# Kernel optimization log

Measured on AMD Instinct MI355X. Metric: run time of the kernel, lower is better.

Reference implementation:

```python
import jax, jax.numpy as jnp
import numpy as np

N_NODES = 50000
N_EDGES = 800000
EMB = 2
HID = 128
DIM = 2
IN_SZ = 3 * DIM + 1 + EMB  # boids_ode: delta_pos, r, dpos_i, dpos_j, a_i
MAX_RADIUS = 0.1


def setup_inputs() -> dict:
    key = jax.random.key(0)
    ks = jax.random.split(key, 12)
    s = 0.05  # modest weight scale for numeric stability
    return {
        "pos": jax.random.uniform(ks[0], (N_NODES, DIM), dtype=jnp.float32),
        "vel": jax.random.normal(ks[1], (N_NODES, DIM), dtype=jnp.float32),
        "a": jax.random.normal(ks[2], (2, N_NODES, EMB), dtype=jnp.float32),
        "vnorm": jnp.ones((1,), dtype=jnp.float32),
        "w0": jax.random.normal(ks[3], (IN_SZ, HID), dtype=jnp.float32) * s,
        "b0": jnp.zeros((HID,), dtype=jnp.float32),
        "w1": jax.random.normal(ks[4], (HID, HID), dtype=jnp.float32) * s,
        "b1": jnp.zeros((HID,), dtype=jnp.float32),
        "w2": jax.random.normal(ks[5], (HID, HID), dtype=jnp.float32) * s,
        "b2": jnp.zeros((HID,), dtype=jnp.float32),
        "w3": jax.random.normal(ks[6], (HID, HID), dtype=jnp.float32) * s,
        "b3": jnp.zeros((HID,), dtype=jnp.float32),
        "w4": jax.random.normal(ks[7], (HID, 2), dtype=jnp.float32) * s,
        "b4": jnp.zeros((2,), dtype=jnp.float32),
        "edge_index": jax.random.randint(ks[8], (2, N_EDGES), 0, N_NODES, dtype=jnp.int64),
        "data_id": 1,
    }


def _mlp(x, w0, b0, w1, b1, w2, b2, w3, b3, w4, b4):
    # 5-layer MLP with ReLU between linear layers (lin_edge)
    h = jax.nn.relu(x @ w0 + b0)
    h = jax.nn.relu(h @ w1 + b1)
    h = jax.nn.relu(h @ w2 + b2)
    h = jax.nn.relu(h @ w3 + b3)
    return h @ w4 + b4


def reference(pos, vel, a, vnorm, w0, b0, w1, b1, w2, b2, w3, b3, w4, b4,
              edge_index, data_id):
    d_pos = vel / vnorm                     # [N, 2]
    emb = a[data_id]                        # [N, EMB] (cell_id = arange)
    dst = edge_index[0]
    src = edge_index[1]
    delta_pos = (pos[src] - pos[dst]) / MAX_RADIUS          # [E, 2]
    r = jnp.sqrt(jnp.sum(delta_pos * delta_pos, axis=1))    # [E] (already / max_r)
    # boids_ode message: (delta_pos, r, dpos_i, dpos_j, a_i)
    feats = jnp.concatenate(
        [delta_pos, r[:, None], d_pos[dst], d_pos[src], emb[dst]], axis=-1)
    msgs = _mlp(feats, w0, b0, w1, b1, w2, b2, w3, b3, w4, b4)  # [E, 2]
    out = jax.ops.segment_sum(msgs, dst, num_segments=pos.shape[0])  # aggr='add'
    return out
```

## Files before the change

kernel.cpp:

```cpp
#include <hip/hip_runtime.h>
#include <math.h>

typedef _Float16 f16;
typedef __fp16 h2 __attribute__((ext_vector_type(2)));
typedef f16 f16x8 __attribute__((ext_vector_type(8)));
typedef float f32x16 __attribute__((ext_vector_type(16)));

#define LW0 0
#define LW1 16384
#define LW2 32768
#define W0F 49152
#define W4F 51200
#define BIAS16 55296
#define LBIAS 49152
#define LDS_F16 49536

__global__ void zero_f32(float* __restrict__ p, int n) {
    int i = blockIdx.x * blockDim.x + threadIdx.x;
    if (i < n) p[i] = 0.0f;
}

__global__ void prep_weights(const float* __restrict__ w1, const float* __restrict__ w2,
                             const float* __restrict__ w3, const float* __restrict__ w0,
                             const float* __restrict__ b0, const float* __restrict__ b1,
                             const float* __restrict__ b2, const float* __restrict__ b3,
                             const float* __restrict__ w4, f16* __restrict__ ws) {
    int t = blockIdx.x * 256 + threadIdx.x;
    if (t < 49152) {
        int l = t >> 14, rem = t & 16383;
        int fb = rem >> 12, ks = (rem >> 9) & 7, lane = (rem >> 3) & 63, i = rem & 7;
        int g = lane >> 5, ln = lane & 31;
        int F = 32 * (ks >> 1) + (i & 3) + 8 * (2 * (ks & 1) + (i >> 2)) + 4 * g;
        const float* w = (l == 0) ? w1 : (l == 1) ? w2 : w3;
        ws[t] = (f16)w[F * 128 + 32 * fb + ln];
    } else if (t < 51200) {
        int rem = t - 49152;
        int fb = rem >> 9, lane = (rem >> 3) & 63, i = rem & 7;
        int g = lane >> 5, ln = lane & 31;
        int k = 8 * g + i;
        int f = 32 * fb + ln;
        float v = (k < 9) ? w0[k * 128 + f] : (k == 9 ? b0[f] : 0.0f);
        ws[t] = (f16)v;
    } else if (t < 55296) {
        int rem = t - 51200;
        int ks = rem >> 9, lane = (rem >> 3) & 63, i = rem & 7;
        int g = lane >> 5, ln = lane & 31;
        int F = 32 * (ks >> 1) + (i & 3) + 8 * (2 * (ks & 1) + (i >> 2)) + 4 * g;
        ws[t] = (ln < 2) ? (f16)w4[F * 2 + ln] : (f16)0;
    } else if (t < 55680) {
        int m = t - 55296;
        int i = m & 7, g = (m >> 3) & 1, half = (m >> 4) & 1, fb = (m >> 5) & 3, lm = m >> 7;
        const float* bl = (lm == 0) ? b1 : (lm == 1) ? b2 : b3;
        ws[t] = (f16)bl[32 * fb + (i & 3) + 8 * (2 * half + (i >> 2)) + 4 * g];
    }
}

#define MF(w, b, c) __builtin_amdgcn_mfma_f32_32x32x16_f16(w, b, c, 0, 0, 0)

#define ZACC(acc) { _Pragma("unroll") for (int r_ = 0; r_ < 16; ++r_) acc[r_] = 0.0f; }

#define PACKB(dst, acc, b) {                                                   \
    h2 z2; z2[0] = (__fp16)0; z2[1] = (__fp16)0;                               \
    h2 p0 = __builtin_elementwise_max(__builtin_amdgcn_cvt_pkrtz(acc[8*(b)+0], acc[8*(b)+1]), z2); \
    h2 p1 = __builtin_elementwise_max(__builtin_amdgcn_cvt_pkrtz(acc[8*(b)+2], acc[8*(b)+3]), z2); \
    h2 p2 = __builtin_elementwise_max(__builtin_amdgcn_cvt_pkrtz(acc[8*(b)+4], acc[8*(b)+5]), z2); \
    h2 p3 = __builtin_elementwise_max(__builtin_amdgcn_cvt_pkrtz(acc[8*(b)+6], acc[8*(b)+7]), z2); \
    dst[0]=p0[0]; dst[1]=p0[1]; dst[2]=p1[0]; dst[3]=p1[1];                    \
    dst[4]=p2[0]; dst[5]=p2[1]; dst[6]=p3[0]; dst[7]=p3[1]; }

#define PACKBB(dst, acc, b, bias) {                                            \
    h2 z2; z2[0] = (__fp16)0; z2[1] = (__fp16)0;                               \
    const h2* bp_ = (const h2*)&(bias);                                        \
    h2 p0 = __builtin_elementwise_max(__builtin_amdgcn_cvt_pkrtz(acc[8*(b)+0], acc[8*(b)+1]) + bp_[0], z2); \
    h2 p1 = __builtin_elementwise_max(__builtin_amdgcn_cvt_pkrtz(acc[8*(b)+2], acc[8*(b)+3]) + bp_[1], z2); \
    h2 p2 = __builtin_elementwise_max(__builtin_amdgcn_cvt_pkrtz(acc[8*(b)+4], acc[8*(b)+5]) + bp_[2], z2); \
    h2 p3 = __builtin_elementwise_max(__builtin_amdgcn_cvt_pkrtz(acc[8*(b)+6], acc[8*(b)+7]) + bp_[3], z2); \
    dst[0]=p0[0]; dst[1]=p0[1]; dst[2]=p1[0]; dst[3]=p1[1];                    \
    dst[4]=p2[0]; dst[5]=p2[1]; dst[6]=p3[0]; dst[7]=p3[1]; }

#define MIDFB(LBASE, lm, fb, B0,B1,B2,B3,B4,B5,B6,B7, O0, O1) {                \
    f32x16 acc; ZACC(acc);                                                     \
    const f16* wb = lds + (LBASE) + (fb) * 4096 + lane * 8;                    \
    f16x8 w;                                                                   \
    w = *(const f16x8*)(wb + 0*512); acc = MF(w, B0, acc);                     \
    w = *(const f16x8*)(wb + 1*512); acc = MF(w, B1, acc);                     \
    w = *(const f16x8*)(wb + 2*512); acc = MF(w, B2, acc);                     \
    w = *(const f16x8*)(wb + 3*512); acc = MF(w, B3, acc);                     \
    w = *(const f16x8*)(wb + 4*512); acc = MF(w, B4, acc);                     \
    w = *(const f16x8*)(wb + 5*512); acc = MF(w, B5, acc);                     \
    w = *(const f16x8*)(wb + 6*512); acc = MF(w, B6, acc);                     \
    w = *(const f16x8*)(wb + 7*512); acc = MF(w, B7, acc);                     \
    f16x8 bb0 = lbv[((((lm)*4+(fb))*2+0)*2)+g];                                \
    f16x8 bb1 = lbv[((((lm)*4+(fb))*2+1)*2)+g];                                \
    PACKBB(O0, acc, 0, bb0); PACKBB(O1, acc, 1, bb1); }

#define MIDLAYER(LBASE, lm, I0,I1,I2,I3,I4,I5,I6,I7, O0,O1,O2,O3,O4,O5,O6,O7)  \
    MIDFB(LBASE, lm, 0, I0,I1,I2,I3,I4,I5,I6,I7, O0, O1);                      \
    MIDFB(LBASE, lm, 1, I0,I1,I2,I3,I4,I5,I6,I7, O2, O3);                      \
    MIDFB(LBASE, lm, 2, I0,I1,I2,I3,I4,I5,I6,I7, O4, O5);                      \
    MIDFB(LBASE, lm, 3, I0,I1,I2,I3,I4,I5,I6,I7, O6, O7);

#define L0FB(fb, O0, O1) {                                                     \
    f32x16 acc; ZACC(acc);                                                     \
    f16x8 w = w0gv[(fb) * 64 + lane];                                          \
    acc = MF(w, bh, acc); acc = MF(w, blo, acc);                               \
    PACKB(O0, acc, 0); PACKB(O1, acc, 1); }

__launch_bounds__(1024, 4)
__global__ void gnn_mfma(const float* __restrict__ pos, const float* __restrict__ vel,
                         const float* __restrict__ a, const float* __restrict__ vnorm,
                         const float* __restrict__ b4,
                         const int* __restrict__ ei, const int* __restrict__ did,
                         const f16* __restrict__ ws, float* __restrict__ out,
                         int nNodes, int nEdges)
{
    __shared__ __align__(16) f16 lds[LDS_F16];

    const int tid = threadIdx.x;
    const int lane = tid & 63;
    const int wid = tid >> 6;
    const int g = lane >> 5;
    const int c = lane & 31;

    {
        const f16x8* wv = (const f16x8*)ws;
        f16x8* lv = (f16x8*)lds;
        #pragma unroll
        for (int it = 0; it < 6; ++it) lv[it * 1024 + tid] = wv[it * 1024 + tid];
        if (tid < 48) lv[6144 + tid] = wv[6912 + tid];
    }
    __syncthreads();

    const int chunk = blockIdx.x * 16 + wid;
    if (chunk >= ((nEdges + 31) >> 5)) return;

    const f16x8* w0gv = (const f16x8*)(ws + W0F);
    const f16x8* w4gv = (const f16x8*)(ws + W4F);
    const f16x8* lbv  = (const f16x8*)(lds + LBIAS);

    float fx0=0,fx1=0,fx2=0,fx3=0,fx4=0,fx5=0,fx6=0,fx7=0,fx8=0;
    int dsti = 0;
    const int e = chunk * 32 + c;
    if (g == 0 && e < nEdges) {
        dsti = ei[e];
        int srci = ei[nEdges + e];
        float2 pd = ((const float2*)pos)[dsti];
        float2 ps = ((const float2*)pos)[srci];
        float2 vd = ((const float2*)vel)[dsti];
        float2 vs = ((const float2*)vel)[srci];
        const float2* embp = (const float2*)(a + (size_t)did[0] * (size_t)nNodes * 2);
        float2 ae = embp[dsti];
        float invn = 1.0f / vnorm[0];
        fx0 = (ps.x - pd.x) / 0.1f;
        fx1 = (ps.y - pd.y) / 0.1f;
        fx2 = sqrtf(fx0 * fx0 + fx1 * fx1);
        fx3 = vd.x * invn; fx4 = vd.y * invn;
        fx5 = vs.x * invn; fx6 = vs.y * invn;
        fx7 = ae.x; fx8 = ae.y;
    }
    float ay = __shfl(fx8, c);

    f16x8 bh, blo;
    #pragma unroll
    for (int i = 0; i < 8; ++i) { bh[i] = (f16)0; blo[i] = (f16)0; }
    if (g == 0) {
        f16 h;
        h=(f16)fx0; bh[0]=h; blo[0]=(f16)(fx0-(float)h);
        h=(f16)fx1; bh[1]=h; blo[1]=(f16)(fx1-(float)h);
        h=(f16)fx2; bh[2]=h; blo[2]=(f16)(fx2-(float)h);
        h=(f16)fx3; bh[3]=h; blo[3]=(f16)(fx3-(float)h);
        h=(f16)fx4; bh[4]=h; blo[4]=(f16)(fx4-(float)h);
        h=(f16)fx5; bh[5]=h; blo[5]=(f16)(fx5-(float)h);
        h=(f16)fx6; bh[6]=h; blo[6]=(f16)(fx6-(float)h);
        h=(f16)fx7; bh[7]=h; blo[7]=(f16)(fx7-(float)h);
    } else {
        f16 h = (f16)ay; bh[0] = h; blo[0] = (f16)(ay - (float)h);
        bh[1] = (f16)1.0f;
    }

    f16x8 Pa0,Pa1,Pa2,Pa3,Pa4,Pa5,Pa6,Pa7;
    f16x8 Pb0,Pb1,Pb2,Pb3,Pb4,Pb5,Pb6,Pb7;

    L0FB(0, Pa0, Pa1);  L0FB(1, Pa2, Pa3);  L0FB(2, Pa4, Pa5);  L0FB(3, Pa6, Pa7);

    MIDLAYER(LW0, 0, Pa0,Pa1,Pa2,Pa3,Pa4,Pa5,Pa6,Pa7, Pb0,Pb1,Pb2,Pb3,Pb4,Pb5,Pb6,Pb7)
    MIDLAYER(LW1, 1, Pb0,Pb1,Pb2,Pb3,Pb4,Pb5,Pb6,Pb7, Pa0,Pa1,Pa2,Pa3,Pa4,Pa5,Pa6,Pa7)
    MIDLAYER(LW2, 2, Pa0,Pa1,Pa2,Pa3,Pa4,Pa5,Pa6,Pa7, Pb0,Pb1,Pb2,Pb3,Pb4,Pb5,Pb6,Pb7)

    {
        f32x16 acc; ZACC(acc);
        if (g == 0) { acc[0] = b4[0]; acc[1] = b4[1]; }
        f16x8 w;
        w = w4gv[0*64 + lane]; acc = MF(w, Pb0, acc);
        w = w4gv[1*64 + lane]; acc = MF(w, Pb1, acc);
        w = w4gv[2*64 + lane]; acc = MF(w, Pb2, acc);
        w = w4gv[3*64 + lane]; acc = MF(w, Pb3, acc);
        w = w4gv[4*64 + lane]; acc = MF(w, Pb4, acc);
        w = w4gv[5*64 + lane]; acc = MF(w, Pb5, acc);
        w = w4gv[6*64 + lane]; acc = MF(w, Pb6, acc);
        w = w4gv[7*64 + lane]; acc = MF(w, Pb7, acc);
        if (g == 0 && e < nEdges) {
            atomicAdd(&out[2 * dsti],     acc[0]);
            atomicAdd(&out[2 * dsti + 1], acc[1]);
        }
    }
}

extern "C" void kernel_launch(void* const* d_in, const int* in_sizes, int n_in,
                              void* d_out, int out_size, void* d_ws, size_t ws_size,
                              hipStream_t stream) {
    const float* pos   = (const float*)d_in[0];
    const float* vel   = (const float*)d_in[1];
    const float* a     = (const float*)d_in[2];
    const float* vnorm = (const float*)d_in[3];
    const float* w0    = (const float*)d_in[4];
    const float* b0    = (const float*)d_in[5];
    const float* w1    = (const float*)d_in[6];
    const float* b1    = (const float*)d_in[7];
    const float* w2    = (const float*)d_in[8];
    const float* b2    = (const float*)d_in[9];
    const float* w3    = (const float*)d_in[10];
    const float* b3    = (const float*)d_in[11];
    const float* w4    = (const float*)d_in[12];
    const float* b4    = (const float*)d_in[13];
    const int*   ei    = (const int*)d_in[14];
    const int*   did   = (const int*)d_in[15];
    float* out = (float*)d_out;
    f16* ws = (f16*)d_ws;

    int nEdges = in_sizes[14] / 2;
    int nNodes = in_sizes[0] / 2;

    hipLaunchKernelGGL(zero_f32, dim3((out_size + 255) / 256), dim3(256), 0, stream,
                       out, out_size);
    hipLaunchKernelGGL(prep_weights, dim3(218), dim3(256), 0, stream,
                       w1, w2, w3, w0, b0, b1, b2, b3, w4, ws);
    int nChunks = (nEdges + 31) / 32;
    int grid = (nChunks + 15) / 16;
    hipLaunchKernelGGL(gnn_mfma, dim3(grid), dim3(1024), 0, stream,
                       pos, vel, a, vnorm, b4, ei, did, ws, out,
                       nNodes, nEdges);
}
```

Before: 113.6 us.

## Process two 32-edge tiles per wave to reuse LDS weight loads

Each wave now handles 64 edges as two 32-column MFMA tiles (A and B) that share each weight fragment read from LDS, which halves LDS weight traffic per edge. All 64 lanes now gather edge features, and shuffles rearrange them into the two tile layouts. The block shrinks to 512 threads with launch bounds set to 1 block per CU. Doubling the live accumulators and activations raises register pressure and may limit occupancy, and the LDS weight copy is amortised over fewer waves per block.

```diff
diff --git a/kernel.cpp b/kernel.cpp
--- a/kernel.cpp
+++ b/kernel.cpp
@@ -5,6 +5,7 @@
 typedef __fp16 h2 __attribute__((ext_vector_type(2)));
 typedef f16 f16x8 __attribute__((ext_vector_type(8)));
 typedef float f32x16 __attribute__((ext_vector_type(16)));
+typedef unsigned u32;
 
 #define LW0 0
 #define LW1 16384
@@ -56,7 +57,6 @@
 }
 
 #define MF(w, b, c) __builtin_amdgcn_mfma_f32_32x32x16_f16(w, b, c, 0, 0, 0)
-
 #define ZACC(acc) { _Pragma("unroll") for (int r_ = 0; r_ < 16; ++r_) acc[r_] = 0.0f; }
 
 #define PACKB(dst, acc, b) {                                                   \
@@ -78,35 +78,45 @@
     dst[0]=p0[0]; dst[1]=p0[1]; dst[2]=p1[0]; dst[3]=p1[1];                    \
     dst[4]=p2[0]; dst[5]=p2[1]; dst[6]=p3[0]; dst[7]=p3[1]; }
 
-#define MIDFB(LBASE, lm, fb, B0,B1,B2,B3,B4,B5,B6,B7, O0, O1) {                \
-    f32x16 acc; ZACC(acc);                                                     \
+#define MIDFB2(LBASE, lm, fb, IA, IB, OA0, OA1, OB0, OB1) {                    \
+    f32x16 accA; ZACC(accA); f32x16 accB; ZACC(accB);                          \
     const f16* wb = lds + (LBASE) + (fb) * 4096 + lane * 8;                    \
     f16x8 w;                                                                   \
-    w = *(const f16x8*)(wb + 0*512); acc = MF(w, B0, acc);                     \
-    w = *(const f16x8*)(wb + 1*512); acc = MF(w, B1, acc);                     \
-    w = *(const f16x8*)(wb + 2*512); acc = MF(w, B2, acc);                     \
-    w = *(const f16x8*)(wb + 3*512); acc = MF(w, B3, acc);                     \
-    w = *(const f16x8*)(wb + 4*512); acc = MF(w, B4, acc);                     \
-    w = *(const f16x8*)(wb + 5*512); acc = MF(w, B5, acc);                     \
-    w = *(const f16x8*)(wb + 6*512); acc = MF(w, B6, acc);                     \
-    w = *(const f16x8*)(wb + 7*512); acc = MF(w, B7, acc);                     \
+    w = *(const f16x8*)(wb + 0*512); accA = MF(w, IA##0, accA); accB = MF(w, IB##0, accB); \
+    w = *(const f16x8*)(wb + 1*512); accA = MF(w, IA##1, accA); accB = MF(w, IB##1, accB); \
+    w = *(const f16x8*)(wb + 2*512); accA = MF(w, IA##2, accA); accB = MF(w, IB##2, accB); \
+    w = *(const f16x8*)(wb + 3*512); accA = MF(w, IA##3, accA); accB = MF(w, IB##3, accB); \
+    w = *(const f16x8*)(wb + 4*512); accA = MF(w, IA##4, accA); accB = MF(w, IB##4, accB); \
+    w = *(const f16x8*)(wb + 5*512); accA = MF(w, IA##5, accA); accB = MF(w, IB##5, accB); \
+    w = *(const f16x8*)(wb + 6*512); accA = MF(w, IA##6, accA); accB = MF(w, IB##6, accB); \
+    w = *(const f16x8*)(wb + 7*512); accA = MF(w, IA##7, accA); accB = MF(w, IB##7, accB); \
     f16x8 bb0 = lbv[((((lm)*4+(fb))*2+0)*2)+g];                                \
     f16x8 bb1 = lbv[((((lm)*4+(fb))*2+1)*2)+g];                                \
-    PACKBB(O0, acc, 0, bb0); PACKBB(O1, acc, 1, bb1); }
-
-#define MIDLAYER(LBASE, lm, I0,I1,I2,I3,I4,I5,I6,I7, O0,O1,O2,O3,O4,O5,O6,O7)  \
-    MIDFB(LBASE, lm, 0, I0,I1,I2,I3,I4,I5,I6,I7, O0, O1);                      \
-    MIDFB(LBASE, lm, 1, I0,I1,I2,I3,I4,I5,I6,I7, O2, O3);                      \
-    MIDFB(LBASE, lm, 2, I0,I1,I2,I3,I4,I5,I6,I7, O4, O5);                      \
-    MIDFB(LBASE, lm, 3, I0,I1,I2,I3,I4,I5,I6,I7, O6, O7);
-
-#define L0FB(fb, O0, O1) {                                                     \
-    f32x16 acc; ZACC(acc);                                                     \
+    PACKBB(OA0, accA, 0, bb0); PACKBB(OA1, accA, 1, bb1);                      \
+    PACKBB(OB0, accB, 0, bb0); PACKBB(OB1, accB, 1, bb1); }
+
+#define MIDLAYER2(LBASE, lm, IA, IB, OA, OB)                                   \
+    MIDFB2(LBASE, lm, 0, IA, IB, OA##0, OA##1, OB##0, OB##1);                  \
+    MIDFB2(LBASE, lm, 1, IA, IB, OA##2, OA##3, OB##2, OB##3);                  \
+    MIDFB2(LBASE, lm, 2, IA, IB, OA##4, OA##5, OB##4, OB##5);                  \
+    MIDFB2(LBASE, lm, 3, IA, IB, OA##6, OA##7, OB##6, OB##7);
+
+#define L0FB2(fb, OA0, OA1, OB0, OB1) {                                        \
+    f32x16 accA; ZACC(accA); f32x16 accB; ZACC(accB);                          \
     f16x8 w = w0gv[(fb) * 64 + lane];                                          \
-    acc = MF(w, bh, acc); acc = MF(w, blo, acc);                               \
-    PACKB(O0, acc, 0); PACKB(O1, acc, 1); }
-
-__launch_bounds__(1024, 4)
+    accA = MF(w, bhA, accA); accA = MF(w, bloA, accA);                         \
+    accB = MF(w, bhB, accB); accB = MF(w, bloB, accB);                         \
+    PACKB(OA0, accA, 0); PACKB(OA1, accA, 1);                                  \
+    PACKB(OB0, accB, 0); PACKB(OB1, accB, 1); }
+
+union F8U { f16x8 v; u32 d[4]; };
+static __device__ __forceinline__ u32 pk2(f16 a, f16 b) {
+    union { h2 v; u32 u; } c;
+    c.v[0] = (__fp16)a; c.v[1] = (__fp16)b;
+    return c.u;
+}
+
+__launch_bounds__(512, 1)
 __global__ void gnn_mfma(const float* __restrict__ pos, const float* __restrict__ vel,
                          const float* __restrict__ a, const float* __restrict__ vnorm,
                          const float* __restrict__ b4,
@@ -120,28 +130,26 @@
     const int lane = tid & 63;
     const int wid = tid >> 6;
     const int g = lane >> 5;
-    const int c = lane & 31;
+    const int cl = lane & 31;
 
     {
         const f16x8* wv = (const f16x8*)ws;
         f16x8* lv = (f16x8*)lds;
         #pragma unroll
-        for (int it = 0; it < 6; ++it) lv[it * 1024 + tid] = wv[it * 1024 + tid];
+        for (int it = 0; it < 12; ++it) lv[it * 512 + tid] = wv[it * 512 + tid];
         if (tid < 48) lv[6144 + tid] = wv[6912 + tid];
     }
     __syncthreads();
-
-    const int chunk = blockIdx.x * 16 + wid;
-    if (chunk >= ((nEdges + 31) >> 5)) return;
 
     const f16x8* w0gv = (const f16x8*)(ws + W0F);
     const f16x8* w4gv = (const f16x8*)(ws + W4F);
     const f16x8* lbv  = (const f16x8*)(lds + LBIAS);
 
+    const int base = blockIdx.x * 512 + wid * 64;
+    const int e = base + lane;
     float fx0=0,fx1=0,fx2=0,fx3=0,fx4=0,fx5=0,fx6=0,fx7=0,fx8=0;
     int dsti = 0;
-    const int e = chunk * 32 + c;
-    if (g == 0 && e < nEdges) {
+    if (e < nEdges) {
         dsti = ei[e];
         int srci = ei[nEdges + e];
         float2 pd = ((const float2*)pos)[dsti];
@@ -158,50 +166,82 @@
         fx5 = vs.x * invn; fx6 = vs.y * invn;
         fx7 = ae.x; fx8 = ae.y;
     }
-    float ay = __shfl(fx8, c);
-
-    f16x8 bh, blo;
-    #pragma unroll
-    for (int i = 0; i < 8; ++i) { bh[i] = (f16)0; blo[i] = (f16)0; }
-    if (g == 0) {
+
+    F8U X, Xl;
+    {
         f16 h;
-        h=(f16)fx0; bh[0]=h; blo[0]=(f16)(fx0-(float)h);
-        h=(f16)fx1; bh[1]=h; blo[1]=(f16)(fx1-(float)h);
-        h=(f16)fx2; bh[2]=h; blo[2]=(f16)(fx2-(float)h);
-        h=(f16)fx3; bh[3]=h; blo[3]=(f16)(fx3-(float)h);
-        h=(f16)fx4; bh[4]=h; blo[4]=(f16)(fx4-(float)h);
-        h=(f16)fx5; bh[5]=h; blo[5]=(f16)(fx5-(float)h);
-        h=(f16)fx6; bh[6]=h; blo[6]=(f16)(fx6-(float)h);
-        h=(f16)fx7; bh[7]=h; blo[7]=(f16)(fx7-(float)h);
-    } else {
-        f16 h = (f16)ay; bh[0] = h; blo[0] = (f16)(ay - (float)h);
-        bh[1] = (f16)1.0f;
-    }
-
-    f16x8 Pa0,Pa1,Pa2,Pa3,Pa4,Pa5,Pa6,Pa7;
-    f16x8 Pb0,Pb1,Pb2,Pb3,Pb4,Pb5,Pb6,Pb7;
-
-    L0FB(0, Pa0, Pa1);  L0FB(1, Pa2, Pa3);  L0FB(2, Pa4, Pa5);  L0FB(3, Pa6, Pa7);
-
-    MIDLAYER(LW0, 0, Pa0,Pa1,Pa2,Pa3,Pa4,Pa5,Pa6,Pa7, Pb0,Pb1,Pb2,Pb3,Pb4,Pb5,Pb6,Pb7)
-    MIDLAYER(LW1, 1, Pb0,Pb1,Pb2,Pb3,Pb4,Pb5,Pb6,Pb7, Pa0,Pa1,Pa2,Pa3,Pa4,Pa5,Pa6,Pa7)
-    MIDLAYER(LW2, 2, Pa0,Pa1,Pa2,Pa3,Pa4,Pa5,Pa6,Pa7, Pb0,Pb1,Pb2,Pb3,Pb4,Pb5,Pb6,Pb7)
+        h=(f16)fx0; X.v[0]=h; Xl.v[0]=(f16)(fx0-(float)h);
+        h=(f16)fx1; X.v[1]=h; Xl.v[1]=(f16)(fx1-(float)h);
+        h=(f16)fx2; X.v[2]=h; Xl.v[2]=(f16)(fx2-(float)h);
+        h=(f16)fx3; X.v[3]=h; Xl.v[3]=(f16)(fx3-(float)h);
+        h=(f16)fx4; X.v[4]=h; Xl.v[4]=(f16)(fx4-(float)h);
+        h=(f16)fx5; X.v[5]=h; Xl.v[5]=(f16)(fx5-(float)h);
+        h=(f16)fx6; X.v[6]=h; Xl.v[6]=(f16)(fx6-(float)h);
+        h=(f16)fx7; X.v[7]=h; Xl.v[7]=(f16)(fx7-(float)h);
+    }
+    f16 h8 = (f16)fx8;
+    u32 yh = pk2(h8, (f16)1.0f);
+    u32 yl = pk2((f16)(fx8 - (float)h8), (f16)0);
+
+    u32 yhA = (u32)__shfl((int)yh, cl);
+    u32 ylA = (u32)__shfl((int)yl, cl);
+    u32 xb0 = (u32)__shfl((int)X.d[0],  cl + 32);
+    u32 xb1 = (u32)__shfl((int)X.d[1],  cl + 32);
+    u32 xb2 = (u32)__shfl((int)X.d[2],  cl + 32);
+    u32 xb3 = (u32)__shfl((int)X.d[3],  cl + 32);
+    u32 xl0 = (u32)__shfl((int)Xl.d[0], cl + 32);
+    u32 xl1 = (u32)__shfl((int)Xl.d[1], cl + 32);
+    u32 xl2 = (u32)__shfl((int)Xl.d[2], cl + 32);
+    u32 xl3 = (u32)__shfl((int)Xl.d[3], cl + 32);
+    int dB  = __shfl(dsti, cl + 32);
+
+    F8U uA, uAl, uB, uBl;
+    uA.d[0]  = g ? yhA : X.d[0];  uA.d[1]  = g ? 0u : X.d[1];
+    uA.d[2]  = g ? 0u  : X.d[2];  uA.d[3]  = g ? 0u : X.d[3];
+    uAl.d[0] = g ? ylA : Xl.d[0]; uAl.d[1] = g ? 0u : Xl.d[1];
+    uAl.d[2] = g ? 0u  : Xl.d[2]; uAl.d[3] = g ? 0u : Xl.d[3];
+    uB.d[0]  = g ? yh  : xb0;     uB.d[1]  = g ? 0u : xb1;
+    uB.d[2]  = g ? 0u  : xb2;     uB.d[3]  = g ? 0u : xb3;
+    uBl.d[0] = g ? yl  : xl0;     uBl.d[1] = g ? 0u : xl1;
+    uBl.d[2] = g ? 0u  : xl2;     uBl.d[3] = g ? 0u : xl3;
+    f16x8 bhA = uA.v, bloA = uAl.v, bhB = uB.v, bloB = uBl.v;
+
+    f16x8 PaA0,PaA1,PaA2,PaA3,PaA4,PaA5,PaA6,PaA7;
+    f16x8 PaB0,PaB1,PaB2,PaB3,PaB4,PaB5,PaB6,PaB7;
+    f16x8 PbA0,PbA1,PbA2,PbA3,PbA4,PbA5,PbA6,PbA7;
+    f16x8 PbB0,PbB1,PbB2,PbB3,PbB4,PbB5,PbB6,PbB7;
+
+    L0FB2(0, PaA0, PaA1, PaB0, PaB1);
+    L0FB2(1, PaA2, PaA3, PaB2, PaB3);
+    L0FB2(2, PaA4, PaA5, PaB4, PaB5);
+    L0FB2(3, PaA6, PaA7, PaB6, PaB7);
+
+    MIDLAYER2(LW0, 0, PaA, PaB, PbA, PbB)
+    MIDLAYER2(LW1, 1, PbA, PbB, PaA, PaB)
+    MIDLAYER2(LW2, 2, PaA, PaB, PbA, PbB)
 
     {
-        f32x16 acc; ZACC(acc);
-        if (g == 0) { acc[0] = b4[0]; acc[1] = b4[1]; }
+        const float b40 = b4[0], b41 = b4[1];
+        f32x16 accA; ZACC(accA); f32x16 accB; ZACC(accB);
+        if (g == 0) { accA[0] = b40; accA[1] = b41; accB[0] = b40; accB[1] = b41; }
         f16x8 w;
-        w = w4gv[0*64 + lane]; acc = MF(w, Pb0, acc);
-        w = w4gv[1*64 + lane]; acc = MF(w, Pb1, acc);
-        w = w4gv[2*64 + lane]; acc = MF(w, Pb2, acc);
-        w = w4gv[3*64 + lane]; acc = MF(w, Pb3, acc);
-        w = w4gv[4*64 + lane]; acc = MF(w, Pb4, acc);
-        w = w4gv[5*64 + lane]; acc = MF(w, Pb5, acc);
-        w = w4gv[6*64 + lane]; acc = MF(w, Pb6, acc);
-        w = w4gv[7*64 + lane]; acc = MF(w, Pb7, acc);
-        if (g == 0 && e < nEdges) {
-            atomicAdd(&out[2 * dsti],     acc[0]);
-            atomicAdd(&out[2 * dsti + 1], acc[1]);
+        w = w4gv[0*64 + lane]; accA = MF(w, PbA0, accA); accB = MF(w, PbB0, accB);
+        w = w4gv[1*64 + lane]; accA = MF(w, PbA1, accA); accB = MF(w, PbB1, accB);
+        w = w4gv[2*64 + lane]; accA = MF(w, PbA2, accA); accB = MF(w, PbB2, accB);
+        w = w4gv[3*64 + lane]; accA = MF(w, PbA3, accA); accB = MF(w, PbB3, accB);
+        w = w4gv[4*64 + lane]; accA = MF(w, PbA4, accA); accB = MF(w, PbB4, accB);
+        w = w4gv[5*64 + lane]; accA = MF(w, PbA5, accA); accB = MF(w, PbB5, accB);
+        w = w4gv[6*64 + lane]; accA = MF(w, PbA6, accA); accB = MF(w, PbB6, accB);
+        w = w4gv[7*64 + lane]; accA = MF(w, PbA7, accA); accB = MF(w, PbB7, accB);
+        if (g == 0) {
+            if (base + cl < nEdges) {
+                atomicAdd(&out[2 * dsti],     accA[0]);
+                atomicAdd(&out[2 * dsti + 1], accA[1]);
+            }
+            if (base + 32 + cl < nEdges) {
+                atomicAdd(&out[2 * dB],       accB[0]);
+                atomicAdd(&out[2 * dB + 1],   accB[1]);
+            }
         }
     }
 }
@@ -235,9 +275,8 @@
                        out, out_size);
     hipLaunchKernelGGL(prep_weights, dim3(218), dim3(256), 0, stream,
                        w1, w2, w3, w0, b0, b1, b2, b3, w4, ws);
-    int nChunks = (nEdges + 31) / 32;
-    int grid = (nChunks + 15) / 16;
-    hipLaunchKernelGGL(gnn_mfma, dim3(grid), dim3(1024), 0, stream,
+    int grid = (nEdges + 511) / 512;
+    hipLaunchKernelGGL(gnn_mfma, dim3(grid), dim3(512), 0, stream,
                        pos, vel, a, vnorm, b4, ei, did, ws, out,
                        nNodes, nEdges);
 }
```

Measured after the change: 121.2 us. 1.07x slower.
